# Kernel tuning notes

Hardware: AMD Instinct MI355X
Metric: run time of the kernel (lower is better)

The kernel has to match this reference:

```python
import jax, jax.numpy as jnp
import numpy as np

B, N, H = 64, 512, 1024
NH = 8            # attention heads
HD = H // NH      # head dim
STEPS = 24


def setup_inputs() -> dict:
    key = jax.random.key(0)
    ks = jax.random.split(key, 12)
    s = 0.05  # weight scale to keep gates/softmax in a sane range
    return {
        "encoder_outputs": jax.random.normal(ks[0], (B, N, H), dtype=jnp.float32),
        "hidden": jax.random.normal(ks[1], (B, H), dtype=jnp.float32) * s,
        "cell": jax.random.normal(ks[2], (B, H), dtype=jnp.float32) * s,
        "end_node_embed": jax.random.normal(ks[3], (B, H), dtype=jnp.float32),
        "initial_input": jax.random.normal(ks[4], (B, 3 * H), dtype=jnp.float32),
        "max_steps": STEPS,
        # LSTMCell params (torch layout: [4H, in], gate order i,f,g,o)
        "W_ih": jax.random.normal(ks[5], (4 * H, 3 * H), dtype=jnp.float32) * s,
        "b_ih": jnp.zeros((4 * H,), jnp.float32),
        "W_hh": jax.random.normal(ks[6], (4 * H, H), dtype=jnp.float32) * s,
        "b_hh": jnp.zeros((4 * H,), jnp.float32),
        # MultiheadAttention params (torch in_proj [3H,H] = [Wq;Wk;Wv])
        "attn_in_w": jax.random.normal(ks[7], (3 * H, H), dtype=jnp.float32) * s,
        "attn_in_b": jnp.zeros((3 * H,), jnp.float32),
        "attn_out_w": jax.random.normal(ks[8], (H, H), dtype=jnp.float32) * s,
        "attn_out_b": jnp.zeros((H,), jnp.float32),
        # query_transform Linear
        "qt_w": jax.random.normal(ks[9], (H, H), dtype=jnp.float32) * s,
        "qt_b": jnp.zeros((H,), jnp.float32),
    }


def reference(encoder_outputs, hidden, cell, end_node_embed, initial_input,
              max_steps, W_ih, b_ih, W_hh, b_hh,
              attn_in_w, attn_in_b, attn_out_w, attn_out_b, qt_w, qt_b):
    b, n, h = encoder_outputs.shape
    nh, hd = NH, H // NH
    Wq, Wk, Wv = jnp.split(attn_in_w, 3, axis=0)
    bq, bk, bv = jnp.split(attn_in_b, 3)
    S = max_steps
    dt = encoder_outputs.dtype
    buf0 = jnp.zeros((b, S, h), dt)  # preallocated KV cache of decoder hiddens
    neg = jnp.asarray(-1e30, dt)
    scale = 1.0 / jnp.sqrt(jnp.asarray(hd, dt))
    pos = jnp.arange(S)

    def step(carry, t):
        hn, cn, x, buf = carry
        # --- LSTMCell (torch gate order i,f,g,o) ---
        gates = x @ W_ih.T + b_ih + hn @ W_hh.T + b_hh
        i, f, g, o = jnp.split(gates, 4, axis=-1)
        cn = jax.nn.sigmoid(f) * cn + jax.nn.sigmoid(i) * jnp.tanh(g)
        hn = jax.nn.sigmoid(o) * jnp.tanh(cn)
        buf = buf.at[:, t, :].set(hn)
        # --- causal self-attention: q = current hidden, kv = all hiddens <= t ---
        q = (hn @ Wq.T + bq).reshape(b, nh, hd)
        k = (buf @ Wk.T + bk).reshape(b, S, nh, hd)
        v = (buf @ Wv.T + bv).reshape(b, S, nh, hd)
        scores = jnp.einsum('bhd,bshd->bhs', q, k) * scale
        scores = jnp.where((pos > t)[None, None, :], neg, scores)
        attn = jax.nn.softmax(scores, axis=-1)
        ctx = jnp.einsum('bhs,bshd->bhd', attn, v).reshape(b, h)
        attn_out = ctx @ attn_out_w.T + attn_out_b
        # --- pointer scoring ---
        query = (0.5 * (hn + attn_out)) @ qt_w.T + qt_b
        logits = jnp.einsum('bh,bnh->bn', query, encoder_outputs)  # [B,N]
        _, idx = jax.lax.top_k(logits, 3)
        idx = jnp.sort(idx, axis=1)
        top3 = jnp.take_along_axis(encoder_outputs, idx[:, :, None], axis=1)  # [B,3,H]
        x = top3.reshape(b, 3 * h)
        return (hn, cn, x, buf), (logits, idx)

    _, (logits, idx) = jax.lax.scan(
        step, (hidden, cell, initial_input, buf0), jnp.arange(S))
    return logits, idx  # [max_steps,B,N], [max_steps,B,3]
```

## Files before the change

### kernel.cpp

```cpp
#include <hip/hip_runtime.h>
#include <math.h>

#define B_  64
#define N_  512
#define H_  1024
#define NH_ 8
#define HD_ 128
#define S_  24

__global__ __launch_bounds__(256) void wc_pre(
    const float* __restrict__ Wqt, const float* __restrict__ Wout,
    float* __restrict__ W2)
{
  __shared__ float As[16][68];
  __shared__ float Bs[16][68];
  const int tid = threadIdx.x;
  const int k0 = (blockIdx.x & 15) * 64;
  const int n0 = (blockIdx.x >> 4) * 64;
  const int tn = tid & 15, tm = tid >> 4;

#pragma unroll
  for (int i = 0; i < 4; ++i) {
    int n = n0 + tm * 4 + i;
    float4 w = *(const float4*)(Wqt + (size_t)n * 1024 + k0 + tn * 4);
    *(float4*)(W2 + (size_t)n * 2048 + k0 + tn * 4) =
        make_float4(0.5f * w.x, 0.5f * w.y, 0.5f * w.z, 0.5f * w.w);
  }

  float acc[4][4];
#pragma unroll
  for (int i = 0; i < 4; ++i)
#pragma unroll
    for (int j = 0; j < 4; ++j) acc[i][j] = 0.f;

  for (int m0 = 0; m0 < 1024; m0 += 16) {
    {
      int nn = tid >> 2, mm = (tid & 3) * 4;
      float4 a = *(const float4*)(Wqt + (size_t)(n0 + nn) * 1024 + m0 + mm);
      As[mm + 0][nn] = a.x; As[mm + 1][nn] = a.y;
      As[mm + 2][nn] = a.z; As[mm + 3][nn] = a.w;
      int mr = tid >> 4, kc = (tid & 15) * 4;
      float4 b = *(const float4*)(Wout + (size_t)(m0 + mr) * 1024 + k0 + kc);
      *(float4*)(&Bs[mr][kc]) = b;
    }
    __syncthreads();
#pragma unroll
    for (int m = 0; m < 16; ++m) {
      float av[4], bv[4];
      *(float4*)av = *(const float4*)(&As[m][tm * 4]);
      *(float4*)bv = *(const float4*)(&Bs[m][tn * 4]);
#pragma unroll
      for (int i = 0; i < 4; ++i)
#pragma unroll
        for (int j = 0; j < 4; ++j)
          acc[i][j] = fmaf(av[i], bv[j], acc[i][j]);
    }
    __syncthreads();
  }
#pragma unroll
  for (int i = 0; i < 4; ++i) {
    int n = n0 + tm * 4 + i;
    *(float4*)(W2 + (size_t)n * 2048 + 1024 + k0 + tn * 4) =
        make_float4(0.5f * acc[i][0], 0.5f * acc[i][1],
                    0.5f * acc[i][2], 0.5f * acc[i][3]);
  }
}

__global__ __launch_bounds__(256) void bc_pre(
    const float* __restrict__ Wqt, const float* __restrict__ bout,
    const float* __restrict__ bqt, float* __restrict__ bc)
{
  int w = threadIdx.x >> 6, lane = threadIdx.x & 63;
  int n = blockIdx.x * 4 + w;
  const float* row = Wqt + (size_t)n * 1024;
  float s = 0.f;
#pragma unroll
  for (int c = 0; c < 4; ++c) {
    float4 a = *(const float4*)(row + lane * 16 + c * 4);
    float4 b = *(const float4*)(bout + lane * 16 + c * 4);
    s = fmaf(a.x, b.x, fmaf(a.y, b.y, fmaf(a.z, b.z, fmaf(a.w, b.w, s))));
  }
#pragma unroll
  for (int off = 32; off > 0; off >>= 1) s += __shfl_down(s, off, 64);
  if (lane == 0) bc[n] = 0.5f * s + bqt[n];
}

__global__ __launch_bounds__(512, 2) void gemm5(
    const float* __restrict__ A0, int ldA0, const float* __restrict__ W0, int ldW0,
    int K0,
    const float* __restrict__ A1, int ldA1, const float* __restrict__ W1, int ldW1,
    const float* __restrict__ enc, const int* __restrict__ idxi, int gather,
    float* __restrict__ P, int N, int KS)
{
  __shared__ float As[16 * 68];
  __shared__ float Bs[16 * 132];
  const int tid = threadIdx.x;
  const int nb = blockIdx.x, sp = blockIdx.y;
  const int ks = sp * KS;

  const float* A; const float* W; int ldA, ldW, koff; int seg0;
  if (ks < K0) { A = A0; W = W0; ldA = ldA0; ldW = ldW0; koff = ks; seg0 = 1; }
  else { A = A1; W = W1; ldA = ldA1; ldW = ldW1; koff = ks - K0; seg0 = 0; }

  const int tn = tid & 31, tm = tid >> 5;
  const int lr = tid >> 2, lc = (tid & 3) * 4;

  float acc[4][4];
#pragma unroll
  for (int i = 0; i < 4; ++i)
#pragma unroll
    for (int j = 0; j < 4; ++j) acc[i][j] = 0.f;

  const float* Wrow = W + (size_t)(nb * 128 + lr) * ldW + koff + lc;
  const float* Arow = nullptr;
  if (tid < 256) {
    if (seg0 && gather) {
      int ei = idxi[lr * 3 + (koff >> 10)];
      Arow = enc + ((size_t)lr * 512 + ei) * 1024 + (koff & 1023) + lc;
    } else {
      Arow = A + (size_t)lr * ldA + koff + lc;
    }
  }

  for (int k0 = 0; k0 < KS; k0 += 16) {
    float4 b4 = *(const float4*)(Wrow + k0);
    if (tid < 256) {
      float4 a4 = *(const float4*)(Arow + k0);
      As[(lc + 0) * 68 + lr] = a4.x; As[(lc + 1) * 68 + lr] = a4.y;
      As[(lc + 2) * 68 + lr] = a4.z; As[(lc + 3) * 68 + lr] = a4.w;
    }
    Bs[(lc + 0) * 132 + lr] = b4.x; Bs[(lc + 1) * 132 + lr] = b4.y;
    Bs[(lc + 2) * 132 + lr] = b4.z; Bs[(lc + 3) * 132 + lr] = b4.w;
    __syncthreads();
#pragma unroll
    for (int k = 0; k < 16; ++k) {
      float av[4], bv[4];
      *(float4*)av = *(const float4*)(As + k * 68 + tm * 4);
      *(float4*)bv = *(const float4*)(Bs + k * 132 + tn * 4);
#pragma unroll
      for (int i = 0; i < 4; ++i)
#pragma unroll
        for (int j = 0; j < 4; ++j)
          acc[i][j] = fmaf(av[i], bv[j], acc[i][j]);
    }
    __syncthreads();
  }
  float* Pb = P + (size_t)sp * 64 * N + nb * 128;
#pragma unroll
  for (int i = 0; i < 4; ++i)
    *(float4*)(Pb + (size_t)(tm * 4 + i) * N + tn * 4) =
        make_float4(acc[i][0], acc[i][1], acc[i][2], acc[i][3]);
}

__device__ __forceinline__ float sigm(float x) { return 1.f / (1.f + expf(-x)); }

__global__ __launch_bounds__(256) void lstm_red(
    const float* __restrict__ P, const float* __restrict__ b_ih,
    const float* __restrict__ b_hh, const float* __restrict__ c_in,
    float* __restrict__ h_out, float* __restrict__ c_out)
{
  int idx = blockIdx.x * 256 + threadIdx.x;
  int b = idx >> 8, j4 = (idx & 255) * 4;
  float g[4][4];
#pragma unroll
  for (int c = 0; c < 4; ++c) {
    int n = c * 1024 + j4;
    float4 s = *(const float4*)(b_ih + n);
    float4 s2 = *(const float4*)(b_hh + n);
    s.x += s2.x; s.y += s2.y; s.z += s2.z; s.w += s2.w;
#pragma unroll
    for (int sp = 0; sp < 8; ++sp) {
      float4 v = *(const float4*)(P + ((size_t)sp * 64 + b) * 4096 + n);
      s.x += v.x; s.y += v.y; s.z += v.z; s.w += v.w;
    }
    g[c][0] = s.x; g[c][1] = s.y; g[c][2] = s.z; g[c][3] = s.w;
  }
  float4 cp = *(const float4*)(c_in + b * 1024 + j4);
  float cv[4] = {cp.x, cp.y, cp.z, cp.w};
  float4 ho, co;
  float* hp = &ho.x; float* cpn = &co.x;
#pragma unroll
  for (int e = 0; e < 4; ++e) {
    float c = sigm(g[1][e]) * cv[e] + sigm(g[0][e]) * tanhf(g[2][e]);
    cpn[e] = c;
    hp[e] = sigm(g[3][e]) * tanhf(c);
  }
  *(float4*)(c_out + b * 1024 + j4) = co;
  *(float4*)(h_out + b * 1024 + j4) = ho;
}

__global__ __launch_bounds__(128) void attn_fused(
    const float* __restrict__ P, const float* __restrict__ bqkv,
    float* __restrict__ Kc, float* __restrict__ Vc,
    float* __restrict__ ctx, int t)
{
  const float scale = 0.08838834764831845f;
  int bh = blockIdx.x;
  int b = bh >> 3, h = bh & 7;
  int d = threadIdx.x;
  __shared__ float qs[128];
  __shared__ float sc[S_];

  const float* Pb = P + (size_t)b * 3072 + h * 128 + d;
  float qv = bqkv[h * 128 + d];
  float kv = bqkv[1024 + h * 128 + d];
  float vv = bqkv[2048 + h * 128 + d];
#pragma unroll
  for (int sp = 0; sp < 8; ++sp) {
    const float* pp = Pb + (size_t)sp * 64 * 3072;
    qv += pp[0]; kv += pp[1024]; vv += pp[2048];
  }
  float* Kb = Kc + (size_t)(b * NH_ + h) * S_ * HD_;
  float* Vb = Vc + (size_t)(b * NH_ + h) * S_ * HD_;
  Kb[t * 128 + d] = kv;
  Vb[t * 128 + d] = vv;
  qs[d] = qv;
  __syncthreads();

  int wave = d >> 6, lane = d & 63;
  for (int s = wave; s <= t; s += 2) {
    float pr = qs[lane] * Kb[s * 128 + lane] + qs[lane + 64] * Kb[s * 128 + lane + 64];
#pragma unroll
    for (int off = 32; off > 0; off >>= 1) pr += __shfl_down(pr, off, 64);
    if (lane == 0) sc[s] = pr * scale;
  }
  __syncthreads();

  float m = -3.4e38f;
  for (int s = 0; s <= t; ++s) m = fmaxf(m, sc[s]);
  float den = 0.f;
  for (int s = 0; s <= t; ++s) den += expf(sc[s] - m);
  float acc = 0.f;
  for (int s = 0; s <= t; ++s) acc += expf(sc[s] - m) * Vb[s * 128 + d];
  ctx[(size_t)b * 1024 + h * 128 + d] = acc / den;
}

__device__ __forceinline__ void ins3(float v, int i,
    float& v0, int& i0, float& v1, int& i1, float& v2, int& i2)
{
  if (v > v0 || (v == v0 && i < i0)) {
    v2 = v1; i2 = i1; v1 = v0; i1 = i0; v0 = v; i0 = i;
  } else if (v > v1 || (v == v1 && i < i1)) {
    v2 = v1; i2 = i1; v1 = v; i1 = i;
  } else if (v > v2 || (v == v2 && i < i2)) {
    v2 = v; i2 = i;
  }
}

__global__ __launch_bounds__(256) void qt_red(
    const float* __restrict__ P, const float* __restrict__ bc,
    float* __restrict__ q)
{
  int idx = blockIdx.x * 256 + threadIdx.x;
  int b = idx >> 8, j4 = (idx & 255) * 4;
  float4 s = *(const float4*)(bc + j4);
#pragma unroll
  for (int sp = 0; sp < 16; ++sp) {
    float4 v = *(const float4*)(P + ((size_t)sp * 64 + b) * 1024 + j4);
    s.x += v.x; s.y += v.y; s.z += v.z; s.w += v.w;
  }
  *(float4*)(q + (size_t)b * 1024 + j4) = s;
}

__global__ __launch_bounds__(256) void logits2(
    const float* __restrict__ q, const float* __restrict__ enc,
    float* __restrict__ out,
    float* __restrict__ candv, int* __restrict__ candi)
{
  __shared__ float sl[16];
  const int blk = blockIdx.x;
  const int b = blk >> 5, ch = blk & 31;
  const int wave = threadIdx.x >> 6, lane = threadIdx.x & 63;

  const float* qb = q + (size_t)b * 1024 + lane * 4;
  float4 qv[4];
#pragma unroll
  for (int i = 0; i < 4; ++i) qv[i] = *(const float4*)(qb + i * 256);

  const float* eb = enc + ((size_t)b * N_ + ch * 16) * 1024 + lane * 4;
#pragma unroll
  for (int r = 0; r < 4; ++r) {
    const int row = wave * 4 + r;
    const float* e = eb + (size_t)row * 1024;
    float s = 0.f;
#pragma unroll
    for (int i = 0; i < 4; ++i) {
      float4 ev = *(const float4*)(e + i * 256);
      s = fmaf(qv[i].x, ev.x, s);
      s = fmaf(qv[i].y, ev.y, s);
      s = fmaf(qv[i].z, ev.z, s);
      s = fmaf(qv[i].w, ev.w, s);
    }
#pragma unroll
    for (int off = 32; off > 0; off >>= 1) s += __shfl_down(s, off, 64);
    if (lane == 0) sl[row] = s;
  }
  __syncthreads();
  if (threadIdx.x < 16)
    out[(size_t)b * N_ + ch * 16 + threadIdx.x] = sl[threadIdx.x];
  if (threadIdx.x == 0) {
    float v0 = -3.4e38f, v1 = -3.4e38f, v2 = -3.4e38f;
    int i0 = 0x7fffffff, i1 = 0x7fffffff, i2 = 0x7fffffff;
#pragma unroll
    for (int k = 0; k < 16; ++k)
      ins3(sl[k], ch * 16 + k, v0, i0, v1, i1, v2, i2);
    candv[blk * 3 + 0] = v0; candi[blk * 3 + 0] = i0;
    candv[blk * 3 + 1] = v1; candi[blk * 3 + 1] = i1;
    candv[blk * 3 + 2] = v2; candi[blk * 3 + 2] = i2;
  }
}

__global__ __launch_bounds__(64) void top3_merge(
    const float* __restrict__ candv, const int* __restrict__ candi,
    float* __restrict__ idx_out, int* __restrict__ idxi)
{
  int b = threadIdx.x;
  float v0 = -3.4e38f, v1 = -3.4e38f, v2 = -3.4e38f;
  int i0 = 0x7fffffff, i1 = 0x7fffffff, i2 = 0x7fffffff;
  for (int q = 0; q < 32; ++q) {
    int base = (b * 32 + q) * 3;
#pragma unroll
    for (int k = 0; k < 3; ++k)
      ins3(candv[base + k], candi[base + k], v0, i0, v1, i1, v2, i2);
  }
  int a = i0, bb = i1, c = i2, tw;
  if (a > bb) { tw = a; a = bb; bb = tw; }
  if (bb > c) { tw = bb; bb = c; c = tw; }
  if (a > bb) { tw = a; a = bb; bb = tw; }
  idxi[b * 3 + 0] = a; idxi[b * 3 + 1] = bb; idxi[b * 3 + 2] = c;
  idx_out[b * 3 + 0] = (float)a;
  idx_out[b * 3 + 1] = (float)bb;
  idx_out[b * 3 + 2] = (float)c;
}

extern "C" void kernel_launch(void* const* d_in, const int* in_sizes, int n_in,
                              void* d_out, int out_size, void* d_ws, size_t ws_size,
                              hipStream_t stream)
{
  (void)in_sizes; (void)n_in; (void)out_size; (void)ws_size;
  const float* enc   = (const float*)d_in[0];
  const float* h0    = (const float*)d_in[1];
  const float* c0    = (const float*)d_in[2];
  const float* x0    = (const float*)d_in[4];
  const float* W_ih  = (const float*)d_in[6];
  const float* b_ih  = (const float*)d_in[7];
  const float* W_hh  = (const float*)d_in[8];
  const float* b_hh  = (const float*)d_in[9];
  const float* Wqkv  = (const float*)d_in[10];
  const float* bqkv  = (const float*)d_in[11];
  const float* Wout  = (const float*)d_in[12];
  const float* bout  = (const float*)d_in[13];
  const float* Wqt   = (const float*)d_in[14];
  const float* bqt   = (const float*)d_in[15];

  float* ws   = (float*)d_ws;
  float* P    = ws;
  float* W2   = P + 8 * 64 * 4096;
  float* bc   = W2 + 1024 * 2048;
  float* hbuf = bc + 1024;
  float* cbuf = hbuf + 64 * 1024;
  float* ctx  = cbuf + 64 * 1024;
  float* Kc   = ctx + 64 * 1024;
  float* Vc   = Kc + 64 * NH_ * S_ * HD_;
  int*   idxi = (int*)(Vc + 64 * NH_ * S_ * HD_);

  float* qbuf  = P + 16 * 64 * 1024;
  float* candv = qbuf + 64 * 1024;
  int*   candi = (int*)(candv + 2048 * 3);

  float* logits_out = (float*)d_out;
  float* idx_out    = logits_out + (size_t)S_ * B_ * N_;

  wc_pre<<<dim3(256), dim3(256), 0, stream>>>(Wqt, Wout, W2);
  bc_pre<<<dim3(256), dim3(256), 0, stream>>>(Wqt, bout, bqt, bc);

  for (int t = 0; t < S_; ++t) {
    const float* xin   = (t == 0) ? x0 : nullptr;
    const float* hprev = (t == 0) ? h0 : hbuf;
    const float* cprev = (t == 0) ? c0 : cbuf;

    gemm5<<<dim3(32, 8), dim3(512), 0, stream>>>(
        xin, 3072, W_ih, 3072, 3072,
        hprev, 1024, W_hh, 1024,
        enc, idxi, t > 0, P, 4096, 512);
    lstm_red<<<dim3(64), dim3(256), 0, stream>>>(P, b_ih, b_hh, cprev, hbuf, cbuf);

    gemm5<<<dim3(24, 8), dim3(512), 0, stream>>>(
        hbuf, 1024, Wqkv, 1024, 1024,
        hbuf, 1024, Wqkv, 1024,
        enc, idxi, 0, P, 3072, 128);
    attn_fused<<<dim3(512), dim3(128), 0, stream>>>(P, bqkv, Kc, Vc, ctx, t);

    gemm5<<<dim3(8, 16), dim3(512), 0, stream>>>(
        hbuf, 1024, W2, 2048, 1024,
        ctx, 1024, W2 + 1024, 2048,
        enc, idxi, 0, P, 1024, 128);
    qt_red<<<dim3(64), dim3(256), 0, stream>>>(P, bc, qbuf);
    logits2<<<dim3(2048), dim3(256), 0, stream>>>(
        qbuf, enc, logits_out + (size_t)t * B_ * N_, candv, candi);
    top3_merge<<<dim3(1), dim3(64), 0, stream>>>(
        candv, candi, idx_out + (size_t)t * B_ * 3, idxi);
  }
}
```

Measured before the change: 4.354 ms.

## Fuse all decoder steps into one persistent kernel with grid barriers

Replaces the 8 kernel launches per step (192 in total) with one persistent 256-block kernel. Each phase (LSTM gemm, gate reduction, QKV gemm, attention, query gemm, reduction, logits, top3 merge) is separated by an atomic grid barrier. This targets launch overhead and inter-kernel gaps. It relies on all 256 blocks being co-resident, otherwise the barriers deadlock, and some phases now run on fewer threads per block.

```diff
diff --git a/kernel.cpp b/kernel.cpp
--- a/kernel.cpp
+++ b/kernel.cpp
@@ -68,8 +68,10 @@
 
 __global__ __launch_bounds__(256) void bc_pre(
     const float* __restrict__ Wqt, const float* __restrict__ bout,
-    const float* __restrict__ bqt, float* __restrict__ bc)
-{
+    const float* __restrict__ bqt, float* __restrict__ bc,
+    unsigned* __restrict__ bar)
+{
+  if (blockIdx.x == 0 && threadIdx.x == 0) bar[0] = 0u;
   int w = threadIdx.x >> 6, lane = threadIdx.x & 63;
   int n = blockIdx.x * 4 + w;
   const float* row = Wqt + (size_t)n * 1024;
@@ -85,43 +87,46 @@
   if (lane == 0) bc[n] = 0.5f * s + bqt[n];
 }
 
-__global__ __launch_bounds__(512, 2) void gemm5(
-    const float* __restrict__ A0, int ldA0, const float* __restrict__ W0, int ldW0,
-    int K0,
-    const float* __restrict__ A1, int ldA1, const float* __restrict__ W1, int ldW1,
-    const float* __restrict__ enc, const int* __restrict__ idxi, int gather,
-    float* __restrict__ P, int N, int KS)
-{
-  __shared__ float As[16 * 68];
-  __shared__ float Bs[16 * 132];
+__device__ __forceinline__ void gridbar(unsigned* bar, unsigned target)
+{
+  __syncthreads();
+  if (threadIdx.x == 0) {
+    __threadfence();
+    __hip_atomic_fetch_add(bar, 1u, __ATOMIC_ACQ_REL, __HIP_MEMORY_SCOPE_AGENT);
+    while (__hip_atomic_load(bar, __ATOMIC_ACQUIRE, __HIP_MEMORY_SCOPE_AGENT) < target)
+      __builtin_amdgcn_s_sleep(1);
+    __threadfence();
+  }
+  __syncthreads();
+}
+
+__device__ __forceinline__ float sigm(float x) { return 1.f / (1.f + expf(-x)); }
+
+__device__ __forceinline__ void ins3(float v, int i,
+    float& v0, int& i0, float& v1, int& i1, float& v2, int& i2)
+{
+  if (v > v0 || (v == v0 && i < i0)) {
+    v2 = v1; i2 = i1; v1 = v0; i1 = i0; v0 = v; i0 = i;
+  } else if (v > v1 || (v == v1 && i < i1)) {
+    v2 = v1; i2 = i1; v1 = v; i1 = i;
+  } else if (v > v2 || (v == v2 && i < i2)) {
+    v2 = v; i2 = i;
+  }
+}
+
+__device__ __forceinline__ void gemm_tile(
+    const float* __restrict__ Arow, const float* __restrict__ Wrow,
+    int KS, int N, int sp, int nb, float* __restrict__ P,
+    float* __restrict__ As, float* __restrict__ Bs)
+{
   const int tid = threadIdx.x;
-  const int nb = blockIdx.x, sp = blockIdx.y;
-  const int ks = sp * KS;
-
-  const float* A; const float* W; int ldA, ldW, koff; int seg0;
-  if (ks < K0) { A = A0; W = W0; ldA = ldA0; ldW = ldW0; koff = ks; seg0 = 1; }
-  else { A = A1; W = W1; ldA = ldA1; ldW = ldW1; koff = ks - K0; seg0 = 0; }
-
   const int tn = tid & 31, tm = tid >> 5;
   const int lr = tid >> 2, lc = (tid & 3) * 4;
-
   float acc[4][4];
 #pragma unroll
   for (int i = 0; i < 4; ++i)
 #pragma unroll
     for (int j = 0; j < 4; ++j) acc[i][j] = 0.f;
-
-  const float* Wrow = W + (size_t)(nb * 128 + lr) * ldW + koff + lc;
-  const float* Arow = nullptr;
-  if (tid < 256) {
-    if (seg0 && gather) {
-      int ei = idxi[lr * 3 + (koff >> 10)];
-      Arow = enc + ((size_t)lr * 512 + ei) * 1024 + (koff & 1023) + lc;
-    } else {
-      Arow = A + (size_t)lr * ldA + koff + lc;
-    }
-  }
-
   for (int k0 = 0; k0 < KS; k0 += 16) {
     float4 b4 = *(const float4*)(Wrow + k0);
     if (tid < 256) {
@@ -152,185 +157,222 @@
         make_float4(acc[i][0], acc[i][1], acc[i][2], acc[i][3]);
 }
 
-__device__ __forceinline__ float sigm(float x) { return 1.f / (1.f + expf(-x)); }
-
-__global__ __launch_bounds__(256) void lstm_red(
-    const float* __restrict__ P, const float* __restrict__ b_ih,
-    const float* __restrict__ b_hh, const float* __restrict__ c_in,
-    float* __restrict__ h_out, float* __restrict__ c_out)
-{
-  int idx = blockIdx.x * 256 + threadIdx.x;
-  int b = idx >> 8, j4 = (idx & 255) * 4;
-  float g[4][4];
-#pragma unroll
-  for (int c = 0; c < 4; ++c) {
-    int n = c * 1024 + j4;
-    float4 s = *(const float4*)(b_ih + n);
-    float4 s2 = *(const float4*)(b_hh + n);
-    s.x += s2.x; s.y += s2.y; s.z += s2.z; s.w += s2.w;
-#pragma unroll
-    for (int sp = 0; sp < 8; ++sp) {
-      float4 v = *(const float4*)(P + ((size_t)sp * 64 + b) * 4096 + n);
-      s.x += v.x; s.y += v.y; s.z += v.z; s.w += v.w;
-    }
-    g[c][0] = s.x; g[c][1] = s.y; g[c][2] = s.z; g[c][3] = s.w;
-  }
-  float4 cp = *(const float4*)(c_in + b * 1024 + j4);
-  float cv[4] = {cp.x, cp.y, cp.z, cp.w};
-  float4 ho, co;
-  float* hp = &ho.x; float* cpn = &co.x;
-#pragma unroll
-  for (int e = 0; e < 4; ++e) {
-    float c = sigm(g[1][e]) * cv[e] + sigm(g[0][e]) * tanhf(g[2][e]);
-    cpn[e] = c;
-    hp[e] = sigm(g[3][e]) * tanhf(c);
-  }
-  *(float4*)(c_out + b * 1024 + j4) = co;
-  *(float4*)(h_out + b * 1024 + j4) = ho;
-}
-
-__global__ __launch_bounds__(128) void attn_fused(
-    const float* __restrict__ P, const float* __restrict__ bqkv,
-    float* __restrict__ Kc, float* __restrict__ Vc,
-    float* __restrict__ ctx, int t)
-{
-  const float scale = 0.08838834764831845f;
-  int bh = blockIdx.x;
-  int b = bh >> 3, h = bh & 7;
-  int d = threadIdx.x;
-  __shared__ float qs[128];
-  __shared__ float sc[S_];
-
-  const float* Pb = P + (size_t)b * 3072 + h * 128 + d;
-  float qv = bqkv[h * 128 + d];
-  float kv = bqkv[1024 + h * 128 + d];
-  float vv = bqkv[2048 + h * 128 + d];
-#pragma unroll
-  for (int sp = 0; sp < 8; ++sp) {
-    const float* pp = Pb + (size_t)sp * 64 * 3072;
-    qv += pp[0]; kv += pp[1024]; vv += pp[2048];
-  }
-  float* Kb = Kc + (size_t)(b * NH_ + h) * S_ * HD_;
-  float* Vb = Vc + (size_t)(b * NH_ + h) * S_ * HD_;
-  Kb[t * 128 + d] = kv;
-  Vb[t * 128 + d] = vv;
-  qs[d] = qv;
-  __syncthreads();
-
-  int wave = d >> 6, lane = d & 63;
-  for (int s = wave; s <= t; s += 2) {
-    float pr = qs[lane] * Kb[s * 128 + lane] + qs[lane + 64] * Kb[s * 128 + lane + 64];
-#pragma unroll
-    for (int off = 32; off > 0; off >>= 1) pr += __shfl_down(pr, off, 64);
-    if (lane == 0) sc[s] = pr * scale;
-  }
-  __syncthreads();
-
-  float m = -3.4e38f;
-  for (int s = 0; s <= t; ++s) m = fmaxf(m, sc[s]);
-  float den = 0.f;
-  for (int s = 0; s <= t; ++s) den += expf(sc[s] - m);
-  float acc = 0.f;
-  for (int s = 0; s <= t; ++s) acc += expf(sc[s] - m) * Vb[s * 128 + d];
-  ctx[(size_t)b * 1024 + h * 128 + d] = acc / den;
-}
-
-__device__ __forceinline__ void ins3(float v, int i,
-    float& v0, int& i0, float& v1, int& i1, float& v2, int& i2)
-{
-  if (v > v0 || (v == v0 && i < i0)) {
-    v2 = v1; i2 = i1; v1 = v0; i1 = i0; v0 = v; i0 = i;
-  } else if (v > v1 || (v == v1 && i < i1)) {
-    v2 = v1; i2 = i1; v1 = v; i1 = i;
-  } else if (v > v2 || (v == v2 && i < i2)) {
-    v2 = v; i2 = i;
-  }
-}
-
-__global__ __launch_bounds__(256) void qt_red(
-    const float* __restrict__ P, const float* __restrict__ bc,
-    float* __restrict__ q)
-{
-  int idx = blockIdx.x * 256 + threadIdx.x;
-  int b = idx >> 8, j4 = (idx & 255) * 4;
-  float4 s = *(const float4*)(bc + j4);
-#pragma unroll
-  for (int sp = 0; sp < 16; ++sp) {
-    float4 v = *(const float4*)(P + ((size_t)sp * 64 + b) * 1024 + j4);
-    s.x += v.x; s.y += v.y; s.z += v.z; s.w += v.w;
-  }
-  *(float4*)(q + (size_t)b * 1024 + j4) = s;
-}
-
-__global__ __launch_bounds__(256) void logits2(
-    const float* __restrict__ q, const float* __restrict__ enc,
-    float* __restrict__ out,
-    float* __restrict__ candv, int* __restrict__ candi)
-{
-  __shared__ float sl[16];
-  const int blk = blockIdx.x;
-  const int b = blk >> 5, ch = blk & 31;
-  const int wave = threadIdx.x >> 6, lane = threadIdx.x & 63;
-
-  const float* qb = q + (size_t)b * 1024 + lane * 4;
-  float4 qv[4];
-#pragma unroll
-  for (int i = 0; i < 4; ++i) qv[i] = *(const float4*)(qb + i * 256);
-
-  const float* eb = enc + ((size_t)b * N_ + ch * 16) * 1024 + lane * 4;
-#pragma unroll
-  for (int r = 0; r < 4; ++r) {
-    const int row = wave * 4 + r;
-    const float* e = eb + (size_t)row * 1024;
-    float s = 0.f;
-#pragma unroll
-    for (int i = 0; i < 4; ++i) {
-      float4 ev = *(const float4*)(e + i * 256);
-      s = fmaf(qv[i].x, ev.x, s);
-      s = fmaf(qv[i].y, ev.y, s);
-      s = fmaf(qv[i].z, ev.z, s);
-      s = fmaf(qv[i].w, ev.w, s);
-    }
-#pragma unroll
-    for (int off = 32; off > 0; off >>= 1) s += __shfl_down(s, off, 64);
-    if (lane == 0) sl[row] = s;
-  }
-  __syncthreads();
-  if (threadIdx.x < 16)
-    out[(size_t)b * N_ + ch * 16 + threadIdx.x] = sl[threadIdx.x];
-  if (threadIdx.x == 0) {
-    float v0 = -3.4e38f, v1 = -3.4e38f, v2 = -3.4e38f;
-    int i0 = 0x7fffffff, i1 = 0x7fffffff, i2 = 0x7fffffff;
-#pragma unroll
-    for (int k = 0; k < 16; ++k)
-      ins3(sl[k], ch * 16 + k, v0, i0, v1, i1, v2, i2);
-    candv[blk * 3 + 0] = v0; candi[blk * 3 + 0] = i0;
-    candv[blk * 3 + 1] = v1; candi[blk * 3 + 1] = i1;
-    candv[blk * 3 + 2] = v2; candi[blk * 3 + 2] = i2;
-  }
-}
-
-__global__ __launch_bounds__(64) void top3_merge(
-    const float* __restrict__ candv, const int* __restrict__ candi,
-    float* __restrict__ idx_out, int* __restrict__ idxi)
-{
-  int b = threadIdx.x;
-  float v0 = -3.4e38f, v1 = -3.4e38f, v2 = -3.4e38f;
-  int i0 = 0x7fffffff, i1 = 0x7fffffff, i2 = 0x7fffffff;
-  for (int q = 0; q < 32; ++q) {
-    int base = (b * 32 + q) * 3;
-#pragma unroll
-    for (int k = 0; k < 3; ++k)
-      ins3(candv[base + k], candi[base + k], v0, i0, v1, i1, v2, i2);
-  }
-  int a = i0, bb = i1, c = i2, tw;
-  if (a > bb) { tw = a; a = bb; bb = tw; }
-  if (bb > c) { tw = bb; bb = c; c = tw; }
-  if (a > bb) { tw = a; a = bb; bb = tw; }
-  idxi[b * 3 + 0] = a; idxi[b * 3 + 1] = bb; idxi[b * 3 + 2] = c;
-  idx_out[b * 3 + 0] = (float)a;
-  idx_out[b * 3 + 1] = (float)bb;
-  idx_out[b * 3 + 2] = (float)c;
+struct DecParams {
+  const float* enc; const float* h0; const float* c0; const float* x0;
+  const float* W_ih; const float* b_ih; const float* W_hh; const float* b_hh;
+  const float* Wqkv; const float* bqkv; const float* W2; const float* bc;
+  float* P; float* hbuf; float* cbuf; float* ctx; float* Kc; float* Vc;
+  float* qbuf; float* candv; int* candi; int* idxi; unsigned* bar;
+  float* logits_out; float* idx_out;
+};
+
+__global__ __launch_bounds__(512, 4) void decoder_all(DecParams p)
+{
+  __shared__ float smem[3200];
+  float* As = smem;
+  float* Bs = smem + 1088;
+  const int bid = blockIdx.x;
+  const int tid = threadIdx.x;
+  const unsigned nblk = gridDim.x;
+  unsigned gen = 0;
+
+  for (int t = 0; t < S_; ++t) {
+    {
+      const int nb = bid & 31, sp = bid >> 5;
+      const int ks = sp * 512;
+      const int lr = tid >> 2, lc = (tid & 3) * 4;
+      const float* W; int ldW, koff; const float* A; int ldA; int gat;
+      if (ks < 3072) { W = p.W_ih; ldW = 3072; koff = ks;
+                       A = p.x0;  ldA = 3072; gat = (t > 0); }
+      else           { W = p.W_hh; ldW = 1024; koff = ks - 3072;
+                       A = (t == 0) ? p.h0 : p.hbuf; ldA = 1024; gat = 0; }
+      const float* Wrow = W + (size_t)(nb * 128 + lr) * ldW + koff + lc;
+      const float* Arow = nullptr;
+      if (tid < 256) {
+        if (gat) {
+          int ei = p.idxi[lr * 3 + (koff >> 10)];
+          Arow = p.enc + ((size_t)lr * 512 + ei) * 1024 + (koff & 1023) + lc;
+        } else {
+          Arow = A + (size_t)lr * ldA + koff + lc;
+        }
+      }
+      gemm_tile(Arow, Wrow, 512, 4096, sp, nb, p.P, As, Bs);
+    }
+    ++gen; gridbar(p.bar, gen * nblk);
+
+    if (tid < 64) {
+      const int item = bid * 64 + tid;
+      const int b = item >> 8, j4 = (item & 255) * 4;
+      const float* cin = (t == 0) ? p.c0 : p.cbuf;
+      float g[4][4];
+#pragma unroll
+      for (int c = 0; c < 4; ++c) {
+        int n = c * 1024 + j4;
+        float4 s = *(const float4*)(p.b_ih + n);
+        float4 s2 = *(const float4*)(p.b_hh + n);
+        s.x += s2.x; s.y += s2.y; s.z += s2.z; s.w += s2.w;
+#pragma unroll
+        for (int sp = 0; sp < 8; ++sp) {
+          float4 v = *(const float4*)(p.P + ((size_t)sp * 64 + b) * 4096 + n);
+          s.x += v.x; s.y += v.y; s.z += v.z; s.w += v.w;
+        }
+        g[c][0] = s.x; g[c][1] = s.y; g[c][2] = s.z; g[c][3] = s.w;
+      }
+      float4 cp = *(const float4*)(cin + b * 1024 + j4);
+      float cv[4] = {cp.x, cp.y, cp.z, cp.w};
+      float4 ho, co; float* hp = &ho.x; float* cpn = &co.x;
+#pragma unroll
+      for (int e = 0; e < 4; ++e) {
+        float c = sigm(g[1][e]) * cv[e] + sigm(g[0][e]) * tanhf(g[2][e]);
+        cpn[e] = c; hp[e] = sigm(g[3][e]) * tanhf(c);
+      }
+      *(float4*)(p.cbuf + b * 1024 + j4) = co;
+      *(float4*)(p.hbuf + b * 1024 + j4) = ho;
+    }
+    ++gen; gridbar(p.bar, gen * nblk);
+
+    if (bid < 192) {
+      const int nb = bid >> 3, sp = bid & 7;
+      const int koff = sp * 128;
+      const int lr = tid >> 2, lc = (tid & 3) * 4;
+      const float* Wrow = p.Wqkv + (size_t)(nb * 128 + lr) * 1024 + koff + lc;
+      const float* Arow = (tid < 256)
+          ? p.hbuf + (size_t)lr * 1024 + koff + lc : nullptr;
+      gemm_tile(Arow, Wrow, 128, 3072, sp, nb, p.P, As, Bs);
+    }
+    ++gen; gridbar(p.bar, gen * nblk);
+
+    if (bid < 128) {
+      const int grp = tid >> 7;
+      const int pair = bid * 4 + grp;
+      const int b = pair >> 3, h = pair & 7, d = tid & 127;
+      float* qs = smem + grp * 160;
+      float* sc = qs + 128;
+      const float scale = 0.08838834764831845f;
+      const float* Pb = p.P + (size_t)b * 3072 + h * 128 + d;
+      float qv = p.bqkv[h * 128 + d];
+      float kv = p.bqkv[1024 + h * 128 + d];
+      float vv = p.bqkv[2048 + h * 128 + d];
+#pragma unroll
+      for (int sp = 0; sp < 8; ++sp) {
+        const float* pp = Pb + (size_t)sp * 64 * 3072;
+        qv += pp[0]; kv += pp[1024]; vv += pp[2048];
+      }
+      float* Kb = p.Kc + (size_t)(b * NH_ + h) * S_ * HD_;
+      float* Vb = p.Vc + (size_t)(b * NH_ + h) * S_ * HD_;
+      Kb[t * 128 + d] = kv;
+      Vb[t * 128 + d] = vv;
+      qs[d] = qv;
+      __syncthreads();
+      int w2 = d >> 6, lane = d & 63;
+      for (int s = w2; s <= t; s += 2) {
+        float pr = qs[lane] * Kb[s * 128 + lane] +
+                   qs[lane + 64] * Kb[s * 128 + lane + 64];
+#pragma unroll
+        for (int off = 32; off > 0; off >>= 1) pr += __shfl_down(pr, off, 64);
+        if (lane == 0) sc[s] = pr * scale;
+      }
+      __syncthreads();
+      float m = -3.4e38f;
+      for (int s = 0; s <= t; ++s) m = fmaxf(m, sc[s]);
+      float den = 0.f;
+      for (int s = 0; s <= t; ++s) den += expf(sc[s] - m);
+      float acc = 0.f;
+      for (int s = 0; s <= t; ++s) acc += expf(sc[s] - m) * Vb[s * 128 + d];
+      p.ctx[(size_t)b * 1024 + h * 128 + d] = acc / den;
+    }
+    ++gen; gridbar(p.bar, gen * nblk);
+
+    if (bid < 128) {
+      const int nb = bid & 7, sp = bid >> 3;
+      const int lr = tid >> 2, lc = (tid & 3) * 4;
+      const float* A; const float* W; int koff;
+      if (sp < 8) { A = p.hbuf; W = p.W2;        koff = sp * 128; }
+      else        { A = p.ctx;  W = p.W2 + 1024; koff = (sp - 8) * 128; }
+      const float* Wrow = W + (size_t)(nb * 128 + lr) * 2048 + koff + lc;
+      const float* Arow = (tid < 256)
+          ? A + (size_t)lr * 1024 + koff + lc : nullptr;
+      gemm_tile(Arow, Wrow, 128, 1024, sp, nb, p.P, As, Bs);
+    }
+    ++gen; gridbar(p.bar, gen * nblk);
+
+    if (tid < 64) {
+      const int item = bid * 64 + tid;
+      const int b = item >> 8, j4 = (item & 255) * 4;
+      float4 s = *(const float4*)(p.bc + j4);
+#pragma unroll
+      for (int sp = 0; sp < 16; ++sp) {
+        float4 v = *(const float4*)(p.P + ((size_t)sp * 64 + b) * 1024 + j4);
+        s.x += v.x; s.y += v.y; s.z += v.z; s.w += v.w;
+      }
+      *(float4*)(p.qbuf + (size_t)b * 1024 + j4) = s;
+    }
+    ++gen; gridbar(p.bar, gen * nblk);
+
+    {
+      const int wave = tid >> 6, lane = tid & 63;
+      const int lb = bid * 8 + wave;
+      const int b = lb >> 5, ch = lb & 31;
+      const float* qb = p.qbuf + (size_t)b * 1024 + lane * 4;
+      float4 q0 = *(const float4*)(qb);
+      float4 q1 = *(const float4*)(qb + 256);
+      float4 q2 = *(const float4*)(qb + 512);
+      float4 q3 = *(const float4*)(qb + 768);
+      const float* eb = p.enc + ((size_t)b * N_ + ch * 16) * 1024 + lane * 4;
+      float v0 = -3.4e38f, v1 = -3.4e38f, v2 = -3.4e38f;
+      int i0 = 0x7fffffff, i1 = 0x7fffffff, i2 = 0x7fffffff;
+      float myout = 0.f;
+      float* lo = p.logits_out + (size_t)t * B_ * N_ + (size_t)b * N_ + ch * 16;
+#pragma unroll 4
+      for (int r = 0; r < 16; ++r) {
+        const float* e = eb + (size_t)r * 1024;
+        float4 e0 = *(const float4*)(e);
+        float4 e1 = *(const float4*)(e + 256);
+        float4 e2 = *(const float4*)(e + 512);
+        float4 e3 = *(const float4*)(e + 768);
+        float s = 0.f;
+        s = fmaf(q0.x, e0.x, s); s = fmaf(q0.y, e0.y, s);
+        s = fmaf(q0.z, e0.z, s); s = fmaf(q0.w, e0.w, s);
+        s = fmaf(q1.x, e1.x, s); s = fmaf(q1.y, e1.y, s);
+        s = fmaf(q1.z, e1.z, s); s = fmaf(q1.w, e1.w, s);
+        s = fmaf(q2.x, e2.x, s); s = fmaf(q2.y, e2.y, s);
+        s = fmaf(q2.z, e2.z, s); s = fmaf(q2.w, e2.w, s);
+        s = fmaf(q3.x, e3.x, s); s = fmaf(q3.y, e3.y, s);
+        s = fmaf(q3.z, e3.z, s); s = fmaf(q3.w, e3.w, s);
+#pragma unroll
+        for (int off = 32; off > 0; off >>= 1) s += __shfl_xor(s, off, 64);
+        if (lane == r) myout = s;
+        ins3(s, ch * 16 + r, v0, i0, v1, i1, v2, i2);
+      }
+      if (lane < 16) lo[lane] = myout;
+      if (lane == 0) {
+        p.candv[lb * 3 + 0] = v0; p.candi[lb * 3 + 0] = i0;
+        p.candv[lb * 3 + 1] = v1; p.candi[lb * 3 + 1] = i1;
+        p.candv[lb * 3 + 2] = v2; p.candi[lb * 3 + 2] = i2;
+      }
+    }
+    ++gen; gridbar(p.bar, gen * nblk);
+
+    if (bid == 0 && tid < 64) {
+      const int b = tid;
+      float v0 = -3.4e38f, v1 = -3.4e38f, v2 = -3.4e38f;
+      int i0 = 0x7fffffff, i1 = 0x7fffffff, i2 = 0x7fffffff;
+      for (int q = 0; q < 32; ++q) {
+        int base = (b * 32 + q) * 3;
+#pragma unroll
+        for (int k = 0; k < 3; ++k)
+          ins3(p.candv[base + k], p.candi[base + k], v0, i0, v1, i1, v2, i2);
+      }
+      int a = i0, bb = i1, c = i2, tw;
+      if (a > bb) { tw = a; a = bb; bb = tw; }
+      if (bb > c) { tw = bb; bb = c; c = tw; }
+      if (a > bb) { tw = a; a = bb; bb = tw; }
+      p.idxi[b * 3 + 0] = a; p.idxi[b * 3 + 1] = bb; p.idxi[b * 3 + 2] = c;
+      float* io = p.idx_out + (size_t)t * B_ * 3 + b * 3;
+      io[0] = (float)a; io[1] = (float)bb; io[2] = (float)c;
+    }
+    ++gen; gridbar(p.bar, gen * nblk);
+  }
 }
 
 extern "C" void kernel_launch(void* const* d_in, const int* in_sizes, int n_in,
@@ -363,6 +405,7 @@
   float* Kc   = ctx + 64 * 1024;
   float* Vc   = Kc + 64 * NH_ * S_ * HD_;
   int*   idxi = (int*)(Vc + 64 * NH_ * S_ * HD_);
+  unsigned* bar = (unsigned*)(idxi + 192);
 
   float* qbuf  = P + 16 * 64 * 1024;
   float* candv = qbuf + 64 * 1024;
@@ -372,33 +415,16 @@
   float* idx_out    = logits_out + (size_t)S_ * B_ * N_;
 
   wc_pre<<<dim3(256), dim3(256), 0, stream>>>(Wqt, Wout, W2);
-  bc_pre<<<dim3(256), dim3(256), 0, stream>>>(Wqt, bout, bqt, bc);
-
-  for (int t = 0; t < S_; ++t) {
-    const float* xin   = (t == 0) ? x0 : nullptr;
-    const float* hprev = (t == 0) ? h0 : hbuf;
-    const float* cprev = (t == 0) ? c0 : cbuf;
-
-    gemm5<<<dim3(32, 8), dim3(512), 0, stream>>>(
-        xin, 3072, W_ih, 3072, 3072,
-        hprev, 1024, W_hh, 1024,
-        enc, idxi, t > 0, P, 4096, 512);
-    lstm_red<<<dim3(64), dim3(256), 0, stream>>>(P, b_ih, b_hh, cprev, hbuf, cbuf);
-
-    gemm5<<<dim3(24, 8), dim3(512), 0, stream>>>(
-        hbuf, 1024, Wqkv, 1024, 1024,
-        hbuf, 1024, Wqkv, 1024,
-        enc, idxi, 0, P, 3072, 128);
-    attn_fused<<<dim3(512), dim3(128), 0, stream>>>(P, bqkv, Kc, Vc, ctx, t);
-
-    gemm5<<<dim3(8, 16), dim3(512), 0, stream>>>(
-        hbuf, 1024, W2, 2048, 1024,
-        ctx, 1024, W2 + 1024, 2048,
-        enc, idxi, 0, P, 1024, 128);
-    qt_red<<<dim3(64), dim3(256), 0, stream>>>(P, bc, qbuf);
-    logits2<<<dim3(2048), dim3(256), 0, stream>>>(
-        qbuf, enc, logits_out + (size_t)t * B_ * N_, candv, candi);
-    top3_merge<<<dim3(1), dim3(64), 0, stream>>>(
-        candv, candi, idx_out + (size_t)t * B_ * 3, idxi);
-  }
-}
+  bc_pre<<<dim3(256), dim3(256), 0, stream>>>(Wqt, bout, bqt, bc, bar);
+
+  DecParams prm;
+  prm.enc = enc; prm.h0 = h0; prm.c0 = c0; prm.x0 = x0;
+  prm.W_ih = W_ih; prm.b_ih = b_ih; prm.W_hh = W_hh; prm.b_hh = b_hh;
+  prm.Wqkv = Wqkv; prm.bqkv = bqkv; prm.W2 = W2; prm.bc = bc;
+  prm.P = P; prm.hbuf = hbuf; prm.cbuf = cbuf; prm.ctx = ctx;
+  prm.Kc = Kc; prm.Vc = Vc; prm.qbuf = qbuf;
+  prm.candv = candv; prm.candi = candi; prm.idxi = idxi; prm.bar = bar;
+  prm.logits_out = logits_out; prm.idx_out = idx_out;
+
+  decoder_all<<<dim3(256), dim3(512), 0, stream>>>(prm);
+}
```

Measured after the change: 15.05 ms. 246% more time.
